# Kernel tuning notes

Hardware: AMD Instinct MI355X
Metric: run time of the kernel (lower is better)

Reference implementation:

```python
import jax, jax.numpy as jnp
import numpy as np

N_NODES = 50000
N_EDGES = 800000
IN_DIM = 128
HID = 64
OUT_DIM = 128
N_GRAPHS = 256


def setup_inputs() -> dict:
    key = jax.random.key(0)
    ks = jax.random.split(key, 8)
    x = jax.random.normal(ks[0], (N_NODES, IN_DIM), dtype=jnp.float32)
    edge_index = jax.random.randint(ks[1], (2, N_EDGES), 0, N_NODES, dtype=jnp.int64)
    batch = jnp.sort(jax.random.randint(ks[2], (N_NODES,), 0, N_GRAPHS, dtype=jnp.int64))
    # Glorot-ish init for GCN weights, zero bias (PyG default bias=True)
    W1 = jax.random.normal(ks[3], (IN_DIM, HID), dtype=jnp.float32) / np.sqrt(IN_DIM)
    b1 = jnp.zeros((HID,), dtype=jnp.float32)
    W2 = jax.random.normal(ks[4], (HID, HID), dtype=jnp.float32) / np.sqrt(HID)
    b2 = jnp.zeros((HID,), dtype=jnp.float32)
    W3 = jax.random.normal(ks[5], (HID, OUT_DIM), dtype=jnp.float32) / np.sqrt(HID)
    b3 = jnp.zeros((OUT_DIM,), dtype=jnp.float32)
    return {"x": x, "edge_index": edge_index, "batch": batch, "num_graphs": N_GRAPHS,
            "W1": W1, "b1": b1, "W2": W2, "b2": b2, "W3": W3, "b3": b3}


def _gcn_norm(edge_index, n_nodes):
    # PyG GCNConv default: add self-loops, symmetric D^{-1/2}(A+I)D^{-1/2} norm.
    loops = jnp.arange(n_nodes, dtype=edge_index.dtype)
    src = jnp.concatenate([edge_index[0], loops])  # [E + N]
    dst = jnp.concatenate([edge_index[1], loops])
    deg = jax.ops.segment_sum(jnp.ones_like(dst, dtype=jnp.float32), dst,
                              num_segments=n_nodes)
    dinv = jnp.where(deg > 0, jax.lax.rsqrt(jnp.maximum(deg, 1.0)), 0.0)
    norm = dinv[src] * dinv[dst]  # [E + N]
    return src, dst, norm


def _gcn_conv(x, W, b, src, dst, norm, n_nodes):
    h = x @ W                                  # [N, F_out] dense GEMM
    msg = h[src] * norm[:, None]               # gather + scale  [E+N, F_out]
    agg = jax.ops.segment_sum(msg, dst, num_segments=n_nodes)
    return agg + b


def reference(x, edge_index, batch, num_graphs, W1, b1, W2, b2, W3, b3):
    n_nodes = x.shape[0]
    src, dst, norm = _gcn_norm(edge_index, n_nodes)
    h = jax.nn.gelu(_gcn_conv(x, W1, b1, src, dst, norm, n_nodes))
    h = jax.nn.gelu(_gcn_conv(h, W2, b2, src, dst, norm, n_nodes))
    h = _gcn_conv(h, W3, b3, src, dst, norm, n_nodes)
    # global_mean_pool over batch segment ids
    sums = jax.ops.segment_sum(h, batch, num_segments=num_graphs)
    counts = jax.ops.segment_sum(jnp.ones((n_nodes,), dtype=h.dtype), batch,
                                 num_segments=num_graphs)
    return sums / jnp.maximum(counts, 1.0)[:, None]
```

## Files before the change

kernel.cpp:

```cpp
#include <hip/hip_runtime.h>
#include <hip/hip_fp16.h>
#include <math.h>

#define N_NODES   50000
#define N_EDGES   800000
#define IN_DIM    128
#define HID       64
#define OUT_DIM   128
#define N_GRAPHS  256
#define MAX_DEG   64
#define HALF_N    25000
#define PARTS     8
#define PSIZE     (N_NODES / PARTS)
#define EPB       4096
#define AGG_NPB   32

typedef _Float16 half8 __attribute__((ext_vector_type(8)));
typedef float floatx4 __attribute__((ext_vector_type(4)));
typedef unsigned int uintx4 __attribute__((ext_vector_type(4)));


__global__ __launch_bounds__(256) void k_build(const int* __restrict__ src,
                                               const int* __restrict__ dst,
                                               int* __restrict__ degA, int* __restrict__ degB,
                                               int* __restrict__ col) {
    int p     = blockIdx.x & (PARTS - 1);
    int chunk = blockIdx.x >> 3;
    int base  = chunk * EPB;
    int lo = p * PSIZE, hi = lo + PSIZE;
#pragma unroll
    for (int j = 0; j < EPB / 256; j++) {
        int e = base + j * 256 + threadIdx.x;
        if (e < N_EDGES) {
            int d = dst[e];
            if (d >= lo && d < hi) {
                int s = src[e];
                if (s < HALF_N) {
                    int pos = atomicAdd(&degA[d], 1);
                    if (pos < MAX_DEG) col[d * MAX_DEG + pos] = s;
                } else {
                    int pos = atomicAdd(&degB[d], 1);
                    if (pos < MAX_DEG) col[d * MAX_DEG + (MAX_DEG - 1 - pos)] = s;
                }
            }
        }
    }
}

__global__ __launch_bounds__(256) void k_prep(const int* __restrict__ degA,
                                              const int* __restrict__ degB,
                                              float* __restrict__ dinv,
                                              const float* __restrict__ W1, __half* __restrict__ Wt1,
                                              const float* __restrict__ W2, __half* __restrict__ Wt2) {
    int blk = blockIdx.x;
    if (blk < 196) {
        int n = blk * 256 + threadIdx.x;
        if (n < N_NODES) dinv[n] = rsqrtf((float)(degA[n] + degB[n] + 1));
    } else if (blk < 200) {
        int idx = (blk - 196) * 256 + threadIdx.x;
        int g = idx >> 6, n = idx & 63;
#pragma unroll
        for (int i = 0; i < 8; i++)
            Wt1[idx * 8 + i] = __float2half(W1[(8 * g + i) * 64 + n]);
    } else {
        int idx = (blk - 200) * 256 + threadIdx.x;
        if (idx < 512) {
            int g = idx >> 6, n = idx & 63;
#pragma unroll
            for (int i = 0; i < 8; i++)
                Wt2[idx * 8 + i] = __float2half(W2[(8 * g + i) * 64 + n]);
        }
    }
}


__global__ __launch_bounds__(256) void k_mfma1(const float* __restrict__ A,
                                               const float* __restrict__ dinv,
                                               const __half* __restrict__ Bp,
                                               __half* __restrict__ C) {
    constexpr int K = IN_DIM, S = K / 32;
    int wv   = threadIdx.x >> 6;
    int lane = threadIdx.x & 63;
    int quad = lane >> 4, l15 = lane & 15;
    int row0 = blockIdx.x * 64 + wv * 16;
    if (row0 >= N_NODES) return;

    half8 bf[S][4];
#pragma unroll
    for (int s = 0; s < S; s++)
#pragma unroll
        for (int j = 0; j < 4; j++)
            bf[s][j] = *(const half8*)(Bp + ((size_t)((4 * s + quad) * 64 + 16 * j + l15)) * 8);

    floatx4 acc[4];
#pragma unroll
    for (int j = 0; j < 4; j++) acc[j] = 0.f;

    int arow = row0 + l15;
    float dv = dinv[arow];
#pragma unroll
    for (int s = 0; s < S; s++) {
        floatx4 xa = __builtin_nontemporal_load((const floatx4*)(A + (size_t)arow * K + 32 * s + quad * 8));
        floatx4 xb = __builtin_nontemporal_load((const floatx4*)(A + (size_t)arow * K + 32 * s + quad * 8 + 4));
        half8 af;
        af[0] = (_Float16)(xa[0] * dv); af[1] = (_Float16)(xa[1] * dv);
        af[2] = (_Float16)(xa[2] * dv); af[3] = (_Float16)(xa[3] * dv);
        af[4] = (_Float16)(xb[0] * dv); af[5] = (_Float16)(xb[1] * dv);
        af[6] = (_Float16)(xb[2] * dv); af[7] = (_Float16)(xb[3] * dv);
#pragma unroll
        for (int j = 0; j < 4; j++)
            acc[j] = __builtin_amdgcn_mfma_f32_16x16x32_f16(af, bf[s][j], acc[j], 0, 0, 0);
    }
#pragma unroll
    for (int j = 0; j < 4; j++)
#pragma unroll
        for (int r = 0; r < 4; r++)
            C[(size_t)(row0 + quad * 4 + r) * 64 + 16 * j + l15] = __float2half(acc[j][r]);
}


__global__ __launch_bounds__(256) void k_mfma2(const __half* __restrict__ A,
                                               const __half* __restrict__ Bp,
                                               __half* __restrict__ C) {
    constexpr int K = HID, S = K / 32;
    int wv   = threadIdx.x >> 6;
    int lane = threadIdx.x & 63;
    int quad = lane >> 4, l15 = lane & 15;
    int row0 = blockIdx.x * 64 + wv * 16;
    if (row0 >= N_NODES) return;

    half8 bf[S][4];
#pragma unroll
    for (int s = 0; s < S; s++)
#pragma unroll
        for (int j = 0; j < 4; j++)
            bf[s][j] = *(const half8*)(Bp + ((size_t)((4 * s + quad) * 64 + 16 * j + l15)) * 8);

    floatx4 acc[4];
#pragma unroll
    for (int j = 0; j < 4; j++) acc[j] = 0.f;

    int arow = row0 + l15;
#pragma unroll
    for (int s = 0; s < S; s++) {
        half8 af = *(const half8*)(A + (size_t)arow * K + 32 * s + quad * 8);
#pragma unroll
        for (int j = 0; j < 4; j++)
            acc[j] = __builtin_amdgcn_mfma_f32_16x16x32_f16(af, bf[s][j], acc[j], 0, 0, 0);
    }
#pragma unroll
    for (int j = 0; j < 4; j++)
#pragma unroll
        for (int r = 0; r < 4; r++)
            C[(size_t)(row0 + quad * 4 + r) * 64 + 16 * j + l15] = __float2half(acc[j][r]);
}


__device__ __forceinline__ void add8(float* acc, uintx4 v) {
    const __half2* h = (const __half2*)&v;
#pragma unroll
    for (int j = 0; j < 4; j++) {
        acc[2 * j]     += __low2float(h[j]);
        acc[2 * j + 1] += __high2float(h[j]);
    }
}

__global__ __launch_bounds__(256) void k_agg(const __half* __restrict__ T,
                                             const int* __restrict__ col,
                                             const int* __restrict__ degA,
                                             const int* __restrict__ degB,
                                             const float* __restrict__ dinv,
                                             const float* __restrict__ b,
                                             __half* __restrict__ OUT, int mode) {
    __shared__ int cols[AGG_NPB][MAX_DEG + 1];
    int base = blockIdx.x * AGG_NPB;

    for (int idx = threadIdx.x; idx < AGG_NPB * MAX_DEG; idx += 256) {
        int r = idx >> 6, j = idx & 63;
        int g = base + r;
        if (g < N_NODES) cols[r][j] = __builtin_nontemporal_load(&col[g * MAX_DEG + j]);
    }
    __syncthreads();

    int lane = threadIdx.x & 63;
    int wv   = threadIdx.x >> 6;
    int q = lane >> 3, t = lane & 7;
    int local = wv * 8 + q;
    int d = base + local;
    if (d >= N_NODES) return;

    int dgA = degA[d]; if (dgA > MAX_DEG) dgA = MAX_DEG;
    int dgB = degB[d]; if (dgB > MAX_DEG) dgB = MAX_DEG;

    float acc[8];
#pragma unroll
    for (int j = 0; j < 8; j++) acc[j] = 0.f;
    add8(acc, *(const uintx4*)(T + (size_t)d * HID + t * 8));

    const int* cl = cols[local];
    int i = 0;
    for (; i + 4 <= dgA; i += 4) {
        int s0 = cl[i], s1 = cl[i + 1], s2 = cl[i + 2], s3 = cl[i + 3];
        uintx4 v0 = *(const uintx4*)(T + (size_t)s0 * HID + t * 8);
        uintx4 v1 = *(const uintx4*)(T + (size_t)s1 * HID + t * 8);
        uintx4 v2 = *(const uintx4*)(T + (size_t)s2 * HID + t * 8);
        uintx4 v3 = *(const uintx4*)(T + (size_t)s3 * HID + t * 8);
        add8(acc, v0); add8(acc, v1); add8(acc, v2); add8(acc, v3);
    }
    for (; i < dgA; i++)
        add8(acc, *(const uintx4*)(T + (size_t)cl[i] * HID + t * 8));
    i = 0;
    for (; i + 4 <= dgB; i += 4) {
        int s0 = cl[MAX_DEG - 1 - i], s1 = cl[MAX_DEG - 2 - i];
        int s2 = cl[MAX_DEG - 3 - i], s3 = cl[MAX_DEG - 4 - i];
        uintx4 v0 = *(const uintx4*)(T + (size_t)s0 * HID + t * 8);
        uintx4 v1 = *(const uintx4*)(T + (size_t)s1 * HID + t * 8);
        uintx4 v2 = *(const uintx4*)(T + (size_t)s2 * HID + t * 8);
        uintx4 v3 = *(const uintx4*)(T + (size_t)s3 * HID + t * 8);
        add8(acc, v0); add8(acc, v1); add8(acc, v2); add8(acc, v3);
    }
    for (; i < dgB; i++)
        add8(acc, *(const uintx4*)(T + (size_t)cl[MAX_DEG - 1 - i] * HID + t * 8));

    float dv = dinv[d];
    float o[8];
#pragma unroll
    for (int j = 0; j < 8; j++) o[j] = acc[j] * dv;
    if (mode == 0) {
#pragma unroll
        for (int j = 0; j < 8; j++) {
            float v = o[j] + b[t * 8 + j];
            float u2 = 0.7978845608028654f * (v + 0.044715f * v * v * v);
            o[j] = 0.5f * v * (1.0f + tanhf(u2)) * dv;
        }
    }
    __half2 hh[4];
#pragma unroll
    for (int j = 0; j < 4; j++) hh[j] = __floats2half2_rn(o[2 * j], o[2 * j + 1]);
    uintx4 st = *(uintx4*)hh;
    __builtin_nontemporal_store(st, (uintx4*)(OUT + (size_t)d * HID + t * 8));
}


__global__ __launch_bounds__(256) void k_pool_out(const __half* __restrict__ A,
                                                  const int* __restrict__ batch,
                                                  const float* __restrict__ W3,
                                                  const float* __restrict__ b3,
                                                  float* __restrict__ out) {
    int g = blockIdx.x;
    int lo = 0, hi = N_NODES;
    while (lo < hi) { int m = (lo + hi) >> 1; if (batch[m] < g) lo = m + 1; else hi = m; }
    int lo2 = lo, hi2 = N_NODES;
    while (lo2 < hi2) { int m = (lo2 + hi2) >> 1; if (batch[m] < g + 1) lo2 = m + 1; else hi2 = m; }
    int start = lo, end = lo2;

    int lane = threadIdx.x & 63;
    int wave = threadIdx.x >> 6;
    float acc = 0.f;
    for (int n = start + wave; n < end; n += 4)
        acc += __half2float(A[(size_t)n * HID + lane]);

    __shared__ float part[4][HID];
    __shared__ float pooled[HID];
    part[wave][lane] = acc;
    __syncthreads();
    if (threadIdx.x < HID)
        pooled[threadIdx.x] = part[0][threadIdx.x] + part[1][threadIdx.x] +
                              part[2][threadIdx.x] + part[3][threadIdx.x];
    __syncthreads();

    if (threadIdx.x < OUT_DIM) {
        float cntf = (float)(end - start);
        float inv = 1.0f / fmaxf(cntf, 1.0f);
        float s = 0.f;
#pragma unroll
        for (int k = 0; k < HID; k++) s += pooled[k] * W3[k * OUT_DIM + threadIdx.x];
        out[g * OUT_DIM + threadIdx.x] = (s + cntf * b3[threadIdx.x]) * inv;
    }
}


extern "C" void kernel_launch(void* const* d_in, const int* in_sizes, int n_in,
                              void* d_out, int out_size, void* d_ws, size_t ws_size,
                              hipStream_t stream) {
    const float* x     = (const float*)d_in[0];
    const int*   ei    = (const int*)d_in[1];
    const int*   batch = (const int*)d_in[2];
    const float* W1    = (const float*)d_in[4];
    const float* b1    = (const float*)d_in[5];
    const float* W2    = (const float*)d_in[6];
    const float* b2    = (const float*)d_in[7];
    const float* W3    = (const float*)d_in[8];
    const float* b3    = (const float*)d_in[9];
    float* out = (float*)d_out;

    const int* esrc = ei;
    const int* edst = ei + N_EDGES;

    int*    degA = (int*)d_ws;
    int*    degB = degA + N_NODES;
    float*  dinv = (float*)(degB + N_NODES);
    int*    col  = (int*)(dinv + N_NODES);
    __half* t    = (__half*)(col + (size_t)N_NODES * MAX_DEG);
    __half* p    = t + (size_t)N_NODES * HID;
    __half* Wt1  = p + (size_t)N_NODES * HID;
    __half* Wt2  = Wt1 + IN_DIM * HID;

    (void)hipMemsetAsync(degA, 0, (size_t)(2 * N_NODES) * 4, stream);

    const int CHUNKS = (N_EDGES + EPB - 1) / EPB;
    k_build<<<CHUNKS * PARTS, 256, 0, stream>>>(esrc, edst, degA, degB, col);
    k_prep<<<202, 256, 0, stream>>>(degA, degB, dinv, W1, Wt1, W2, Wt2);

    const int GB = (N_NODES + 63) / 64;
    const int AB = (N_NODES + AGG_NPB - 1) / AGG_NPB;

    k_mfma1<<<GB, 256, 0, stream>>>(x, dinv, Wt1, t);
    k_agg<<<AB, 256, 0, stream>>>(t, col, degA, degB, dinv, b1, p, 0);
    k_mfma2<<<GB, 256, 0, stream>>>(p, Wt2, t);
    k_agg<<<AB, 256, 0, stream>>>(t, col, degA, degB, dinv, b2, p, 0);
    k_agg<<<AB, 256, 0, stream>>>(p, col, degA, degB, dinv, b3, t, 1);
    k_pool_out<<<N_GRAPHS, 256, 0, stream>>>(t, batch, W3, b3, out);
}
```

Measured before the change: 237.2 us.

## Fuse all GCN stages into one cooperative persistent kernel with grid syncs

Replaces the memset and seven separate kernel launches with a single cooperative persistent kernel. Stages are separated by grid-wide barriers and each stage loops over its tiles with a grid-stride. The two per-source-half degree counters are merged into one, and the aggregation inner loop is unrolled by 8. This removes launch gaps and tail effects, at the cost of grid.sync overhead and a fixed grid size of up to 4 blocks per CU that may leave stages under-occupied or limit register use.

```diff
diff --git a/kernel.cpp b/kernel.cpp
--- a/kernel.cpp
+++ b/kernel.cpp
@@ -1,6 +1,9 @@
 #include <hip/hip_runtime.h>
+#include <hip/hip_cooperative_groups.h>
 #include <hip/hip_fp16.h>
 #include <math.h>
+
+namespace cg = cooperative_groups;
 
 #define N_NODES   50000
 #define N_EDGES   800000
@@ -9,152 +12,21 @@
 #define OUT_DIM   128
 #define N_GRAPHS  256
 #define MAX_DEG   64
-#define HALF_N    25000
-#define PARTS     8
-#define PSIZE     (N_NODES / PARTS)
-#define EPB       4096
 #define AGG_NPB   32
+#define NB_MFMA   ((N_NODES + 63) / 64)
+#define NB_AGG    ((N_NODES + AGG_NPB - 1) / AGG_NPB)
 
 typedef _Float16 half8 __attribute__((ext_vector_type(8)));
 typedef float floatx4 __attribute__((ext_vector_type(4)));
 typedef unsigned int uintx4 __attribute__((ext_vector_type(4)));
 
-
-__global__ __launch_bounds__(256) void k_build(const int* __restrict__ src,
-                                               const int* __restrict__ dst,
-                                               int* __restrict__ degA, int* __restrict__ degB,
-                                               int* __restrict__ col) {
-    int p     = blockIdx.x & (PARTS - 1);
-    int chunk = blockIdx.x >> 3;
-    int base  = chunk * EPB;
-    int lo = p * PSIZE, hi = lo + PSIZE;
-#pragma unroll
-    for (int j = 0; j < EPB / 256; j++) {
-        int e = base + j * 256 + threadIdx.x;
-        if (e < N_EDGES) {
-            int d = dst[e];
-            if (d >= lo && d < hi) {
-                int s = src[e];
-                if (s < HALF_N) {
-                    int pos = atomicAdd(&degA[d], 1);
-                    if (pos < MAX_DEG) col[d * MAX_DEG + pos] = s;
-                } else {
-                    int pos = atomicAdd(&degB[d], 1);
-                    if (pos < MAX_DEG) col[d * MAX_DEG + (MAX_DEG - 1 - pos)] = s;
-                }
-            }
-        }
-    }
-}
-
-__global__ __launch_bounds__(256) void k_prep(const int* __restrict__ degA,
-                                              const int* __restrict__ degB,
-                                              float* __restrict__ dinv,
-                                              const float* __restrict__ W1, __half* __restrict__ Wt1,
-                                              const float* __restrict__ W2, __half* __restrict__ Wt2) {
-    int blk = blockIdx.x;
-    if (blk < 196) {
-        int n = blk * 256 + threadIdx.x;
-        if (n < N_NODES) dinv[n] = rsqrtf((float)(degA[n] + degB[n] + 1));
-    } else if (blk < 200) {
-        int idx = (blk - 196) * 256 + threadIdx.x;
-        int g = idx >> 6, n = idx & 63;
-#pragma unroll
-        for (int i = 0; i < 8; i++)
-            Wt1[idx * 8 + i] = __float2half(W1[(8 * g + i) * 64 + n]);
-    } else {
-        int idx = (blk - 200) * 256 + threadIdx.x;
-        if (idx < 512) {
-            int g = idx >> 6, n = idx & 63;
-#pragma unroll
-            for (int i = 0; i < 8; i++)
-                Wt2[idx * 8 + i] = __float2half(W2[(8 * g + i) * 64 + n]);
-        }
-    }
-}
-
-
-__global__ __launch_bounds__(256) void k_mfma1(const float* __restrict__ A,
-                                               const float* __restrict__ dinv,
-                                               const __half* __restrict__ Bp,
-                                               __half* __restrict__ C) {
-    constexpr int K = IN_DIM, S = K / 32;
-    int wv   = threadIdx.x >> 6;
-    int lane = threadIdx.x & 63;
-    int quad = lane >> 4, l15 = lane & 15;
-    int row0 = blockIdx.x * 64 + wv * 16;
-    if (row0 >= N_NODES) return;
-
-    half8 bf[S][4];
-#pragma unroll
-    for (int s = 0; s < S; s++)
-#pragma unroll
-        for (int j = 0; j < 4; j++)
-            bf[s][j] = *(const half8*)(Bp + ((size_t)((4 * s + quad) * 64 + 16 * j + l15)) * 8);
-
-    floatx4 acc[4];
-#pragma unroll
-    for (int j = 0; j < 4; j++) acc[j] = 0.f;
-
-    int arow = row0 + l15;
-    float dv = dinv[arow];
-#pragma unroll
-    for (int s = 0; s < S; s++) {
-        floatx4 xa = __builtin_nontemporal_load((const floatx4*)(A + (size_t)arow * K + 32 * s + quad * 8));
-        floatx4 xb = __builtin_nontemporal_load((const floatx4*)(A + (size_t)arow * K + 32 * s + quad * 8 + 4));
-        half8 af;
-        af[0] = (_Float16)(xa[0] * dv); af[1] = (_Float16)(xa[1] * dv);
-        af[2] = (_Float16)(xa[2] * dv); af[3] = (_Float16)(xa[3] * dv);
-        af[4] = (_Float16)(xb[0] * dv); af[5] = (_Float16)(xb[1] * dv);
-        af[6] = (_Float16)(xb[2] * dv); af[7] = (_Float16)(xb[3] * dv);
-#pragma unroll
-        for (int j = 0; j < 4; j++)
-            acc[j] = __builtin_amdgcn_mfma_f32_16x16x32_f16(af, bf[s][j], acc[j], 0, 0, 0);
-    }
-#pragma unroll
-    for (int j = 0; j < 4; j++)
-#pragma unroll
-        for (int r = 0; r < 4; r++)
-            C[(size_t)(row0 + quad * 4 + r) * 64 + 16 * j + l15] = __float2half(acc[j][r]);
-}
-
-
-__global__ __launch_bounds__(256) void k_mfma2(const __half* __restrict__ A,
-                                               const __half* __restrict__ Bp,
-                                               __half* __restrict__ C) {
-    constexpr int K = HID, S = K / 32;
-    int wv   = threadIdx.x >> 6;
-    int lane = threadIdx.x & 63;
-    int quad = lane >> 4, l15 = lane & 15;
-    int row0 = blockIdx.x * 64 + wv * 16;
-    if (row0 >= N_NODES) return;
-
-    half8 bf[S][4];
-#pragma unroll
-    for (int s = 0; s < S; s++)
-#pragma unroll
-        for (int j = 0; j < 4; j++)
-            bf[s][j] = *(const half8*)(Bp + ((size_t)((4 * s + quad) * 64 + 16 * j + l15)) * 8);
-
-    floatx4 acc[4];
-#pragma unroll
-    for (int j = 0; j < 4; j++) acc[j] = 0.f;
-
-    int arow = row0 + l15;
-#pragma unroll
-    for (int s = 0; s < S; s++) {
-        half8 af = *(const half8*)(A + (size_t)arow * K + 32 * s + quad * 8);
-#pragma unroll
-        for (int j = 0; j < 4; j++)
-            acc[j] = __builtin_amdgcn_mfma_f32_16x16x32_f16(af, bf[s][j], acc[j], 0, 0, 0);
-    }
-#pragma unroll
-    for (int j = 0; j < 4; j++)
-#pragma unroll
-        for (int r = 0; r < 4; r++)
-            C[(size_t)(row0 + quad * 4 + r) * 64 + 16 * j + l15] = __float2half(acc[j][r]);
-}
-
+struct Params {
+    const float* x; const int* esrc; const int* edst; const int* batch;
+    const float* W1; const float* b1; const float* W2; const float* b2;
+    const float* W3; const float* b3; float* out;
+    int* deg; float* dinv; int* col;
+    __half* t; __half* p; __half* Wt1; __half* Wt2;
+};
 
 __device__ __forceinline__ void add8(float* acc, uintx4 v) {
     const __half2* h = (const __half2*)&v;
@@ -165,160 +37,263 @@
     }
 }
 
-__global__ __launch_bounds__(256) void k_agg(const __half* __restrict__ T,
-                                             const int* __restrict__ col,
-                                             const int* __restrict__ degA,
-                                             const int* __restrict__ degB,
-                                             const float* __restrict__ dinv,
-                                             const float* __restrict__ b,
-                                             __half* __restrict__ OUT, int mode) {
-    __shared__ int cols[AGG_NPB][MAX_DEG + 1];
-    int base = blockIdx.x * AGG_NPB;
-
-    for (int idx = threadIdx.x; idx < AGG_NPB * MAX_DEG; idx += 256) {
-        int r = idx >> 6, j = idx & 63;
-        int g = base + r;
-        if (g < N_NODES) cols[r][j] = __builtin_nontemporal_load(&col[g * MAX_DEG + j]);
-    }
-    __syncthreads();
-
-    int lane = threadIdx.x & 63;
-    int wv   = threadIdx.x >> 6;
+__device__ void mfma1_stage(const float* __restrict__ A, const float* __restrict__ dinv,
+                            const __half* __restrict__ Bp, __half* __restrict__ C) {
+    constexpr int S = IN_DIM / 32;
+    int tid = threadIdx.x;
+    int wv = tid >> 6, lane = tid & 63, quad = lane >> 4, l15 = lane & 15;
+    half8 bf[S][4];
+#pragma unroll
+    for (int s = 0; s < S; s++)
+#pragma unroll
+        for (int j = 0; j < 4; j++)
+            bf[s][j] = *(const half8*)(Bp + ((size_t)((4 * s + quad) * 64 + 16 * j + l15)) * 8);
+    for (int tile = blockIdx.x; tile < NB_MFMA; tile += gridDim.x) {
+        int row0 = tile * 64 + wv * 16;
+        if (row0 < N_NODES) {
+            floatx4 acc[4];
+#pragma unroll
+            for (int j = 0; j < 4; j++) acc[j] = 0.f;
+            int arow = row0 + l15;
+            float dv = dinv[arow];
+#pragma unroll
+            for (int s = 0; s < S; s++) {
+                floatx4 xa = __builtin_nontemporal_load((const floatx4*)(A + (size_t)arow * IN_DIM + 32 * s + quad * 8));
+                floatx4 xb = __builtin_nontemporal_load((const floatx4*)(A + (size_t)arow * IN_DIM + 32 * s + quad * 8 + 4));
+                half8 af;
+                af[0] = (_Float16)(xa[0] * dv); af[1] = (_Float16)(xa[1] * dv);
+                af[2] = (_Float16)(xa[2] * dv); af[3] = (_Float16)(xa[3] * dv);
+                af[4] = (_Float16)(xb[0] * dv); af[5] = (_Float16)(xb[1] * dv);
+                af[6] = (_Float16)(xb[2] * dv); af[7] = (_Float16)(xb[3] * dv);
+#pragma unroll
+                for (int j = 0; j < 4; j++)
+                    acc[j] = __builtin_amdgcn_mfma_f32_16x16x32_f16(af, bf[s][j], acc[j], 0, 0, 0);
+            }
+#pragma unroll
+            for (int j = 0; j < 4; j++)
+#pragma unroll
+                for (int r = 0; r < 4; r++)
+                    C[(size_t)(row0 + quad * 4 + r) * 64 + 16 * j + l15] = __float2half(acc[j][r]);
+        }
+    }
+}
+
+__device__ void mfma2_stage(const __half* __restrict__ A, const __half* __restrict__ Bp,
+                            __half* __restrict__ C) {
+    constexpr int S = HID / 32;
+    int tid = threadIdx.x;
+    int wv = tid >> 6, lane = tid & 63, quad = lane >> 4, l15 = lane & 15;
+    half8 bf[S][4];
+#pragma unroll
+    for (int s = 0; s < S; s++)
+#pragma unroll
+        for (int j = 0; j < 4; j++)
+            bf[s][j] = *(const half8*)(Bp + ((size_t)((4 * s + quad) * 64 + 16 * j + l15)) * 8);
+    for (int tile = blockIdx.x; tile < NB_MFMA; tile += gridDim.x) {
+        int row0 = tile * 64 + wv * 16;
+        if (row0 < N_NODES) {
+            floatx4 acc[4];
+#pragma unroll
+            for (int j = 0; j < 4; j++) acc[j] = 0.f;
+            int arow = row0 + l15;
+#pragma unroll
+            for (int s = 0; s < S; s++) {
+                half8 af = *(const half8*)(A + (size_t)arow * HID + 32 * s + quad * 8);
+#pragma unroll
+                for (int j = 0; j < 4; j++)
+                    acc[j] = __builtin_amdgcn_mfma_f32_16x16x32_f16(af, bf[s][j], acc[j], 0, 0, 0);
+            }
+#pragma unroll
+            for (int j = 0; j < 4; j++)
+#pragma unroll
+                for (int r = 0; r < 4; r++)
+                    C[(size_t)(row0 + quad * 4 + r) * 64 + 16 * j + l15] = __float2half(acc[j][r]);
+        }
+    }
+}
+
+__device__ void agg_stage(const __half* __restrict__ T, const int* __restrict__ col,
+                          const int* __restrict__ deg, const float* __restrict__ dinv,
+                          const float* __restrict__ bias, __half* __restrict__ OUT,
+                          int mode, int (*cols)[MAX_DEG + 1]) {
+    int tid = threadIdx.x;
+    int lane = tid & 63, wv = tid >> 6;
     int q = lane >> 3, t = lane & 7;
     int local = wv * 8 + q;
-    int d = base + local;
-    if (d >= N_NODES) return;
-
-    int dgA = degA[d]; if (dgA > MAX_DEG) dgA = MAX_DEG;
-    int dgB = degB[d]; if (dgB > MAX_DEG) dgB = MAX_DEG;
-
-    float acc[8];
-#pragma unroll
-    for (int j = 0; j < 8; j++) acc[j] = 0.f;
-    add8(acc, *(const uintx4*)(T + (size_t)d * HID + t * 8));
-
-    const int* cl = cols[local];
-    int i = 0;
-    for (; i + 4 <= dgA; i += 4) {
-        int s0 = cl[i], s1 = cl[i + 1], s2 = cl[i + 2], s3 = cl[i + 3];
-        uintx4 v0 = *(const uintx4*)(T + (size_t)s0 * HID + t * 8);
-        uintx4 v1 = *(const uintx4*)(T + (size_t)s1 * HID + t * 8);
-        uintx4 v2 = *(const uintx4*)(T + (size_t)s2 * HID + t * 8);
-        uintx4 v3 = *(const uintx4*)(T + (size_t)s3 * HID + t * 8);
-        add8(acc, v0); add8(acc, v1); add8(acc, v2); add8(acc, v3);
-    }
-    for (; i < dgA; i++)
-        add8(acc, *(const uintx4*)(T + (size_t)cl[i] * HID + t * 8));
-    i = 0;
-    for (; i + 4 <= dgB; i += 4) {
-        int s0 = cl[MAX_DEG - 1 - i], s1 = cl[MAX_DEG - 2 - i];
-        int s2 = cl[MAX_DEG - 3 - i], s3 = cl[MAX_DEG - 4 - i];
-        uintx4 v0 = *(const uintx4*)(T + (size_t)s0 * HID + t * 8);
-        uintx4 v1 = *(const uintx4*)(T + (size_t)s1 * HID + t * 8);
-        uintx4 v2 = *(const uintx4*)(T + (size_t)s2 * HID + t * 8);
-        uintx4 v3 = *(const uintx4*)(T + (size_t)s3 * HID + t * 8);
-        add8(acc, v0); add8(acc, v1); add8(acc, v2); add8(acc, v3);
-    }
-    for (; i < dgB; i++)
-        add8(acc, *(const uintx4*)(T + (size_t)cl[MAX_DEG - 1 - i] * HID + t * 8));
-
-    float dv = dinv[d];
-    float o[8];
-#pragma unroll
-    for (int j = 0; j < 8; j++) o[j] = acc[j] * dv;
-    if (mode == 0) {
-#pragma unroll
-        for (int j = 0; j < 8; j++) {
-            float v = o[j] + b[t * 8 + j];
-            float u2 = 0.7978845608028654f * (v + 0.044715f * v * v * v);
-            o[j] = 0.5f * v * (1.0f + tanhf(u2)) * dv;
-        }
-    }
-    __half2 hh[4];
-#pragma unroll
-    for (int j = 0; j < 4; j++) hh[j] = __floats2half2_rn(o[2 * j], o[2 * j + 1]);
-    uintx4 st = *(uintx4*)hh;
-    __builtin_nontemporal_store(st, (uintx4*)(OUT + (size_t)d * HID + t * 8));
-}
-
-
-__global__ __launch_bounds__(256) void k_pool_out(const __half* __restrict__ A,
-                                                  const int* __restrict__ batch,
-                                                  const float* __restrict__ W3,
-                                                  const float* __restrict__ b3,
-                                                  float* __restrict__ out) {
-    int g = blockIdx.x;
-    int lo = 0, hi = N_NODES;
-    while (lo < hi) { int m = (lo + hi) >> 1; if (batch[m] < g) lo = m + 1; else hi = m; }
-    int lo2 = lo, hi2 = N_NODES;
-    while (lo2 < hi2) { int m = (lo2 + hi2) >> 1; if (batch[m] < g + 1) lo2 = m + 1; else hi2 = m; }
-    int start = lo, end = lo2;
-
-    int lane = threadIdx.x & 63;
-    int wave = threadIdx.x >> 6;
-    float acc = 0.f;
-    for (int n = start + wave; n < end; n += 4)
-        acc += __half2float(A[(size_t)n * HID + lane]);
-
+    for (int w = blockIdx.x; w < NB_AGG; w += gridDim.x) {
+        __syncthreads();
+        int base = w * AGG_NPB;
+        for (int idx = tid; idx < AGG_NPB * MAX_DEG; idx += 256) {
+            int r = idx >> 6, j = idx & 63, g = base + r;
+            if (g < N_NODES) cols[r][j] = __builtin_nontemporal_load(&col[g * MAX_DEG + j]);
+        }
+        __syncthreads();
+        int d = base + local;
+        if (d < N_NODES) {
+            int dg = deg[d]; if (dg > MAX_DEG) dg = MAX_DEG;
+            float acc[8];
+#pragma unroll
+            for (int j = 0; j < 8; j++) acc[j] = 0.f;
+            add8(acc, *(const uintx4*)(T + (size_t)d * HID + t * 8));
+            const int* cl = cols[local];
+            int i = 0;
+            for (; i + 8 <= dg; i += 8) {
+                uintx4 v[8];
+#pragma unroll
+                for (int u = 0; u < 8; u++)
+                    v[u] = *(const uintx4*)(T + (size_t)cl[i + u] * HID + t * 8);
+#pragma unroll
+                for (int u = 0; u < 8; u++) add8(acc, v[u]);
+            }
+            for (; i + 2 <= dg; i += 2) {
+                uintx4 v0 = *(const uintx4*)(T + (size_t)cl[i] * HID + t * 8);
+                uintx4 v1 = *(const uintx4*)(T + (size_t)cl[i + 1] * HID + t * 8);
+                add8(acc, v0); add8(acc, v1);
+            }
+            if (i < dg)
+                add8(acc, *(const uintx4*)(T + (size_t)cl[i] * HID + t * 8));
+
+            float dv = dinv[d];
+            float o[8];
+#pragma unroll
+            for (int j = 0; j < 8; j++) o[j] = acc[j] * dv;
+            if (mode == 0) {
+#pragma unroll
+                for (int j = 0; j < 8; j++) {
+                    float v = o[j] + bias[t * 8 + j];
+                    float u2 = 0.7978845608028654f * (v + 0.044715f * v * v * v);
+                    o[j] = 0.5f * v * (1.0f + tanhf(u2)) * dv;
+                }
+            }
+            __half2 hh[4];
+#pragma unroll
+            for (int j = 0; j < 4; j++) hh[j] = __floats2half2_rn(o[2 * j], o[2 * j + 1]);
+            uintx4 st = *(uintx4*)hh;
+            __builtin_nontemporal_store(st, (uintx4*)(OUT + (size_t)d * HID + t * 8));
+        }
+    }
+}
+
+__device__ void pool_stage(const __half* __restrict__ A, const int* __restrict__ batch,
+                           const float* __restrict__ W3, const float* __restrict__ b3,
+                           float* __restrict__ out, float (*part)[HID], float* pooled) {
+    int tid = threadIdx.x;
+    int lane = tid & 63, wave = tid >> 6;
+    for (int g = blockIdx.x; g < N_GRAPHS; g += gridDim.x) {
+        __syncthreads();
+        int lo = 0, hi = N_NODES;
+        while (lo < hi) { int m = (lo + hi) >> 1; if (batch[m] < g) lo = m + 1; else hi = m; }
+        int lo2 = lo, hi2 = N_NODES;
+        while (lo2 < hi2) { int m = (lo2 + hi2) >> 1; if (batch[m] < g + 1) lo2 = m + 1; else hi2 = m; }
+        int start = lo, end = lo2;
+        float acc = 0.f;
+        for (int n = start + wave; n < end; n += 4)
+            acc += __half2float(A[(size_t)n * HID + lane]);
+        part[wave][lane] = acc;
+        __syncthreads();
+        if (tid < HID)
+            pooled[tid] = part[0][tid] + part[1][tid] + part[2][tid] + part[3][tid];
+        __syncthreads();
+        if (tid < OUT_DIM) {
+            float cntf = (float)(end - start);
+            float inv = 1.0f / fmaxf(cntf, 1.0f);
+            float s = 0.f;
+#pragma unroll
+            for (int k = 0; k < HID; k++) s += pooled[k] * W3[k * OUT_DIM + tid];
+            out[g * OUT_DIM + tid] = (s + cntf * b3[tid]) * inv;
+        }
+    }
+}
+
+
+__global__ __launch_bounds__(256, 4) void mega(Params P) {
+    __shared__ int cols[AGG_NPB][MAX_DEG + 1];
     __shared__ float part[4][HID];
     __shared__ float pooled[HID];
-    part[wave][lane] = acc;
-    __syncthreads();
-    if (threadIdx.x < HID)
-        pooled[threadIdx.x] = part[0][threadIdx.x] + part[1][threadIdx.x] +
-                              part[2][threadIdx.x] + part[3][threadIdx.x];
-    __syncthreads();
-
-    if (threadIdx.x < OUT_DIM) {
-        float cntf = (float)(end - start);
-        float inv = 1.0f / fmaxf(cntf, 1.0f);
-        float s = 0.f;
-#pragma unroll
-        for (int k = 0; k < HID; k++) s += pooled[k] * W3[k * OUT_DIM + threadIdx.x];
-        out[g * OUT_DIM + threadIdx.x] = (s + cntf * b3[threadIdx.x]) * inv;
-    }
+    cg::grid_group grid = cg::this_grid();
+    int tid  = threadIdx.x;
+    int gtid = blockIdx.x * 256 + tid;
+    int gsz  = gridDim.x * 256;
+
+    for (int i = gtid; i < N_NODES; i += gsz) P.deg[i] = 0;
+    grid.sync();
+
+    {
+        int prt = blockIdx.x & 7, chunk = blockIdx.x >> 3;
+        int chunks = gridDim.x >> 3;
+        int epb = (N_EDGES + chunks - 1) / chunks;
+        int base = chunk * epb;
+        int lim = base + epb; if (lim > N_EDGES) lim = N_EDGES;
+        int lo = prt * (N_NODES / 8), hi = lo + (N_NODES / 8);
+        for (int e = base + tid; e < lim; e += 256) {
+            int d = P.edst[e];
+            if (d >= lo && d < hi) {
+                int s = P.esrc[e];
+                int pos = atomicAdd(&P.deg[d], 1);
+                if (pos < MAX_DEG) P.col[d * MAX_DEG + pos] = s;
+            }
+        }
+    }
+    grid.sync();
+
+    for (int n = gtid; n < N_NODES; n += gsz)
+        P.dinv[n] = rsqrtf((float)(P.deg[n] + 1));
+    if (gtid < (IN_DIM / 8) * 64) {
+        int g2 = gtid >> 6, n = gtid & 63;
+#pragma unroll
+        for (int i = 0; i < 8; i++)
+            P.Wt1[gtid * 8 + i] = __float2half(P.W1[(8 * g2 + i) * 64 + n]);
+    }
+    if (gtid < (HID / 8) * 64) {
+        int g2 = gtid >> 6, n = gtid & 63;
+#pragma unroll
+        for (int i = 0; i < 8; i++)
+            P.Wt2[gtid * 8 + i] = __float2half(P.W2[(8 * g2 + i) * 64 + n]);
+    }
+    grid.sync();
+
+    mfma1_stage(P.x, P.dinv, P.Wt1, P.t);
+    grid.sync();
+    agg_stage(P.t, P.col, P.deg, P.dinv, P.b1, P.p, 0, cols);
+    grid.sync();
+    mfma2_stage(P.p, P.Wt2, P.t);
+    grid.sync();
+    agg_stage(P.t, P.col, P.deg, P.dinv, P.b2, P.p, 0, cols);
+    grid.sync();
+    agg_stage(P.p, P.col, P.deg, P.dinv, P.b3, P.t, 1, cols);
+    grid.sync();
+    pool_stage(P.t, P.batch, P.W3, P.b3, P.out, part, pooled);
 }
 
 
 extern "C" void kernel_launch(void* const* d_in, const int* in_sizes, int n_in,
                               void* d_out, int out_size, void* d_ws, size_t ws_size,
                               hipStream_t stream) {
-    const float* x     = (const float*)d_in[0];
-    const int*   ei    = (const int*)d_in[1];
-    const int*   batch = (const int*)d_in[2];
-    const float* W1    = (const float*)d_in[4];
-    const float* b1    = (const float*)d_in[5];
-    const float* W2    = (const float*)d_in[6];
-    const float* b2    = (const float*)d_in[7];
-    const float* W3    = (const float*)d_in[8];
-    const float* b3    = (const float*)d_in[9];
-    float* out = (float*)d_out;
-
-    const int* esrc = ei;
-    const int* edst = ei + N_EDGES;
-
-    int*    degA = (int*)d_ws;
-    int*    degB = degA + N_NODES;
-    float*  dinv = (float*)(degB + N_NODES);
-    int*    col  = (int*)(dinv + N_NODES);
-    __half* t    = (__half*)(col + (size_t)N_NODES * MAX_DEG);
-    __half* p    = t + (size_t)N_NODES * HID;
-    __half* Wt1  = p + (size_t)N_NODES * HID;
-    __half* Wt2  = Wt1 + IN_DIM * HID;
-
-    (void)hipMemsetAsync(degA, 0, (size_t)(2 * N_NODES) * 4, stream);
-
-    const int CHUNKS = (N_EDGES + EPB - 1) / EPB;
-    k_build<<<CHUNKS * PARTS, 256, 0, stream>>>(esrc, edst, degA, degB, col);
-    k_prep<<<202, 256, 0, stream>>>(degA, degB, dinv, W1, Wt1, W2, Wt2);
-
-    const int GB = (N_NODES + 63) / 64;
-    const int AB = (N_NODES + AGG_NPB - 1) / AGG_NPB;
-
-    k_mfma1<<<GB, 256, 0, stream>>>(x, dinv, Wt1, t);
-    k_agg<<<AB, 256, 0, stream>>>(t, col, degA, degB, dinv, b1, p, 0);
-    k_mfma2<<<GB, 256, 0, stream>>>(p, Wt2, t);
-    k_agg<<<AB, 256, 0, stream>>>(t, col, degA, degB, dinv, b2, p, 0);
-    k_agg<<<AB, 256, 0, stream>>>(p, col, degA, degB, dinv, b3, t, 1);
-    k_pool_out<<<N_GRAPHS, 256, 0, stream>>>(t, batch, W3, b3, out);
-}
+    Params P;
+    P.x     = (const float*)d_in[0];
+    const int* ei = (const int*)d_in[1];
+    P.esrc  = ei;
+    P.edst  = ei + N_EDGES;
+    P.batch = (const int*)d_in[2];
+    P.W1 = (const float*)d_in[4]; P.b1 = (const float*)d_in[5];
+    P.W2 = (const float*)d_in[6]; P.b2 = (const float*)d_in[7];
+    P.W3 = (const float*)d_in[8]; P.b3 = (const float*)d_in[9];
+    P.out = (float*)d_out;
+
+    P.deg  = (int*)d_ws;
+    P.dinv = (float*)(P.deg + N_NODES);
+    P.col  = (int*)(P.dinv + N_NODES);
+    P.t    = (__half*)(P.col + (size_t)N_NODES * MAX_DEG);
+    P.p    = P.t + (size_t)N_NODES * HID;
+    P.Wt1  = P.p + (size_t)N_NODES * HID;
+    P.Wt2  = P.Wt1 + IN_DIM * HID;
+
+    int nb = 0;
+    (void)hipOccupancyMaxActiveBlocksPerMultiprocessor(&nb, mega, 256, 0);
+    if (nb < 1) nb = 1;
+    if (nb > 4) nb = 4;
+    int grid = nb * 256;
+
+    void* args[] = { (void*)&P };
+    (void)hipLaunchCooperativeKernel(mega, dim3(grid), dim3(256), args, 0, stream);
+}
```

Measured after the change: 782.4 us. +229.8%, slower.
